# Kernel tuning notes

Measured on AMD Instinct MI355X. Metric: run time of the kernel, lower is better.

## Reference

```python
import jax, jax.numpy as jnp
import numpy as np

BINS = 10          # init kwarg `bins`
LOSS_WEIGHT = 1.0  # init kwarg `loss_weight`


def setup_inputs() -> dict:
    key = jax.random.key(0)
    k1, k2, k3 = jax.random.split(key, 3)
    B, C = 131072, 80  # [batch_num(anchors), class_num]
    pred = jax.random.normal(k1, (B, C), dtype=jnp.float32)
    target = jax.random.randint(k2, (B, C), 0, 2).astype(jnp.int32)
    label_weight = jax.random.randint(k3, (B, C), 0, 2).astype(jnp.int32)
    return {"pred": pred, "target": target, "label_weight": label_weight}


def _ghmc_loss(pred, target_f, valid_f):
    # total number of valid samples (>=1), matches max(valid.sum().item(), 1.0)
    total = jnp.maximum(valid_f.sum(), 1.0)

    # gradient magnitude g = |sigmoid(pred).detach() - target|, in [0, 1]
    g = jnp.abs(jax.nn.sigmoid(jax.lax.stop_gradient(pred)) - target_f)

    # bin index: edges are i/bins, last edge padded by 1e-6, so
    # floor(g * bins) clipped to [0, bins-1] reproduces the torch loop's
    # per-element assignment (elements exactly on an edge take the later bin,
    # matching the sequential overwrite of weights[inds]).
    bin_idx = jnp.clip(jnp.floor(g * BINS).astype(jnp.int32), 0, BINS - 1)

    # histogram of valid elements per bin (invalid routed to extra bin BINS)
    flat_idx = jnp.where(valid_f > 0, bin_idx, BINS).reshape(-1)
    counts = jnp.bincount(flat_idx, length=BINS + 1)[:BINS].astype(pred.dtype)

    # n = number of non-empty bins (>=1 whenever any element is valid)
    n = jnp.maximum((counts > 0).sum(), 1).astype(pred.dtype)

    # per-bin weight total/num_in_bin, zero for empty bins, then /n
    w_bin = jnp.where(counts > 0, total / jnp.maximum(counts, 1.0), 0.0) / n
    weights = jnp.where(valid_f > 0, w_bin[bin_idx], 0.0)
    weights = jax.lax.stop_gradient(weights)  # histogram weights are detached

    # weighted BCE-with-logits, reduction='sum', then / total
    bce = target_f * jax.nn.softplus(-pred) + (1.0 - target_f) * jax.nn.softplus(pred)
    return (weights * bce).sum() / total * LOSS_WEIGHT


def reference(pred, target, label_weight):
    target_f = target.astype(pred.dtype)
    valid_f = (label_weight > 0).astype(pred.dtype)
    return _ghmc_loss(pred, target_f, valid_f)
```

## Files before the change

### kernel.cpp

```cpp
#include <hip/hip_runtime.h>

#define BINS 10
#define TPB  256
#define NB_MAX 2048
#define FTPB 1024

__global__ __launch_bounds__(TPB, 4) void ghmc_hist_kernel(
    const float4* __restrict__ pred4,
    const int4*   __restrict__ tgt4,
    const int4*   __restrict__ lw4,
    float* __restrict__ part,
    int n4, int n)
{
    float acc_s[BINS];
#pragma unroll
    for (int b = 0; b < BINS; ++b) acc_s[b] = 0.f;
    unsigned long long cA = 0ull, cB = 0ull;

    auto proc = [&](float p, int t, int w) {
        float q   = __int_as_float(__float_as_int(p) ^ (int)((unsigned)t << 31));
        float e   = __expf(-fabsf(q));
        float d   = 1.f + e;
        float r   = __builtin_amdgcn_rcpf(d);
        float sig = (q >= 0.f) ? r : e * r;
        int bin   = (int)(sig * 10.f);
        bin = bin > (BINS - 1) ? (BINS - 1) : bin;
        bool valid = (w > 0);
        float bce = fmaxf(q, 0.f) + __logf(d);
        int binm  = valid ? bin : 255;
#pragma unroll
        for (int b = 0; b < BINS; ++b)
            acc_s[b] += (binm == b) ? bce : 0.f;
        unsigned long long inc = valid ? (1ull << (12 * (bin >> 1))) : 0ull;
        bool odd = (bin & 1) != 0;
        cA += odd ? 0ull : inc;
        cB += odd ? inc  : 0ull;
    };

    const int tid    = threadIdx.x;
    const int stride = gridDim.x * TPB;

    int iA = blockIdx.x * TPB + tid;
    bool vA = iA < n4;
    float4 pA; int4 tA, wA;
    if (vA) { pA = pred4[iA]; tA = tgt4[iA]; wA = lw4[iA]; }
    while (vA) {
        const int iB = iA + stride;
        const bool vB = iB < n4;
        float4 pB; int4 tB, wB;
        if (vB) { pB = pred4[iB]; tB = tgt4[iB]; wB = lw4[iB]; }

        proc(pA.x, tA.x, wA.x); proc(pA.y, tA.y, wA.y);
        proc(pA.z, tA.z, wA.z); proc(pA.w, tA.w, wA.w);

        iA = iB + stride;
        vA = iA < n4;
        if (vA) { pA = pred4[iA]; tA = tgt4[iA]; wA = lw4[iA]; }

        if (vB) {
            proc(pB.x, tB.x, wB.x); proc(pB.y, tB.y, wB.y);
            proc(pB.z, tB.z, wB.z); proc(pB.w, tB.w, wB.w);
        }
    }
    {
        const float* predf = (const float*)pred4;
        const int*   tgtf  = (const int*)tgt4;
        const int*   lwf   = (const int*)lw4;
        for (int j = n4 * 4 + blockIdx.x * TPB + tid; j < n; j += stride)
            proc(predf[j], tgtf[j], lwf[j]);
    }

    float cnt[BINS];
#pragma unroll
    for (int b = 0; b < BINS; ++b) {
        unsigned long long pk = (b & 1) ? cB : cA;
        cnt[b] = (float)((pk >> (12 * (b >> 1))) & 0xFFFull);
    }

#pragma unroll
    for (int b = 0; b < BINS; ++b) {
#pragma unroll
        for (int off = 1; off <= 8; off <<= 1) {
            acc_s[b] += __shfl_xor(acc_s[b], off, 64);
            cnt[b]   += __shfl_xor(cnt[b],   off, 64);
        }
    }

    __shared__ float red[2 * BINS][16];
    const int grp = tid >> 4;
    if ((tid & 15) == 0) {
#pragma unroll
        for (int b = 0; b < BINS; ++b) {
            red[b][grp]        = acc_s[b];
            red[BINS + b][grp] = cnt[b];
        }
    }
    __syncthreads();
    if (tid < 2 * BINS) {
        float v = 0.f;
#pragma unroll
        for (int g = 0; g < 16; ++g) v += red[tid][g];
        part[blockIdx.x * (2 * BINS) + tid] = v;
    }
}

__global__ __launch_bounds__(FTPB) void ghmc_final_kernel(
    const float* __restrict__ part, float* __restrict__ out, int nb)
{
    float acc[2 * BINS];
#pragma unroll
    for (int v = 0; v < 2 * BINS; ++v) acc[v] = 0.f;

    const int tid = threadIdx.x;
    for (int i = tid; i < nb; i += FTPB) {
        const float4* rec = (const float4*)(part + (size_t)i * (2 * BINS));
        float4 a = rec[0], b = rec[1], c = rec[2], d = rec[3], e = rec[4];
        acc[0]  += a.x; acc[1]  += a.y; acc[2]  += a.z; acc[3]  += a.w;
        acc[4]  += b.x; acc[5]  += b.y; acc[6]  += b.z; acc[7]  += b.w;
        acc[8]  += c.x; acc[9]  += c.y; acc[10] += c.z; acc[11] += c.w;
        acc[12] += d.x; acc[13] += d.y; acc[14] += d.z; acc[15] += d.w;
        acc[16] += e.x; acc[17] += e.y; acc[18] += e.z; acc[19] += e.w;
    }

#pragma unroll
    for (int v = 0; v < 2 * BINS; ++v) {
#pragma unroll
        for (int off = 1; off <= 32; off <<= 1)
            acc[v] += __shfl_xor(acc[v], off, 64);
    }

    __shared__ float sh[2 * BINS][16];
    const int wv = tid >> 6, lane = tid & 63;
    if (lane == 0) {
#pragma unroll
        for (int v = 0; v < 2 * BINS; ++v) sh[v][wv] = acc[v];
    }
    __syncthreads();
    if (tid < 2 * BINS) {
        float s = 0.f;
#pragma unroll
        for (int g = 0; g < 16; ++g) s += sh[tid][g];
        sh[tid][0] = s;
    }
    __syncthreads();

    if (tid == 0) {
        float ti = 0.f; int nbn = 0;
        float cnts[BINS];
#pragma unroll
        for (int b = 0; b < BINS; ++b) {
            cnts[b] = sh[BINS + b][0];
            ti += cnts[b];
            nbn += (cnts[b] > 0.f) ? 1 : 0;
        }
        float total = fmaxf(ti, 1.f);
        float nf    = (float)(nbn > 0 ? nbn : 1);
        float loss  = 0.f;
#pragma unroll
        for (int b = 0; b < BINS; ++b) {
            if (cnts[b] > 0.f) {
                float w = (total / cnts[b]) / nf;
                loss += w * sh[b][0];
            }
        }
        out[0] = loss / total * 1.0f;
    }
}

extern "C" void kernel_launch(void* const* d_in, const int* in_sizes, int n_in,
                              void* d_out, int out_size, void* d_ws, size_t ws_size,
                              hipStream_t stream)
{
    const float4* pred4 = (const float4*)d_in[0];
    const int4*   tgt4  = (const int4*)d_in[1];
    const int4*   lw4   = (const int4*)d_in[2];

    const int n  = in_sizes[0];
    const int n4 = n / 4;

    int nb = (n4 + TPB - 1) / TPB;
    if (nb > NB_MAX) nb = NB_MAX;
    int ws_cap = (int)(ws_size / (2 * BINS * sizeof(float)));
    if (nb > ws_cap) nb = ws_cap;
    if (nb < 1) nb = 1;

    float* part = (float*)d_ws;

    ghmc_hist_kernel<<<nb, TPB, 0, stream>>>(pred4, tgt4, lw4, part, n4, n);
    ghmc_final_kernel<<<1, FTPB, 0, stream>>>(part, (float*)d_out, nb);
}
```

Baseline: 40.97 us.

## Pack per-bin counts into float sum accumulators and restructure the streaming loop

Each valid element now adds its BCE value plus a 4096 offset into a single per-bin float accumulator. Counts and sums are recovered afterwards by floor-dividing by the offset, which removes the separate 64-bit packed counters and their selects. Bin selection uses a shift-and-mask of the value's bits instead of a compare-select. The grid-stride loop is rewritten with a precomputed iteration count, a software-prefetched body unrolled by two, and single-pass tail handling. The risk is precision: large offsets in a float accumulator lose low-order bits of the BCE sums, and any BCE above 4096 would corrupt the count recovery.

```diff
diff --git a/kernel.cpp b/kernel.cpp
--- a/kernel.cpp
+++ b/kernel.cpp
@@ -4,6 +4,7 @@
 #define TPB  256
 #define NB_MAX 2048
 #define FTPB 1024
+#define KPACK 4096.0f
 
 __global__ __launch_bounds__(TPB, 4) void ghmc_hist_kernel(
     const float4* __restrict__ pred4,
@@ -12,77 +13,82 @@
     float* __restrict__ part,
     int n4, int n)
 {
-    float acc_s[BINS];
+    float acc[BINS];
 #pragma unroll
-    for (int b = 0; b < BINS; ++b) acc_s[b] = 0.f;
-    unsigned long long cA = 0ull, cB = 0ull;
+    for (int b = 0; b < BINS; ++b) acc[b] = 0.f;
 
     auto proc = [&](float p, int t, int w) {
-        float q   = __int_as_float(__float_as_int(p) ^ (int)((unsigned)t << 31));
-        float e   = __expf(-fabsf(q));
-        float d   = 1.f + e;
-        float r   = __builtin_amdgcn_rcpf(d);
-        float sig = (q >= 0.f) ? r : e * r;
-        int bin   = (int)(sig * 10.f);
+        float q    = __int_as_float(__float_as_int(p) ^ (t << 31));
+        float e    = __expf(-fabsf(q));
+        float d    = 1.f + e;
+        float r    = __builtin_amdgcn_rcpf(d);
+        float num  = (q >= 0.f) ? 1.0f : e;
+        float sig10 = num * (10.f * r);
+        int bin    = (int)sig10;
         bin = bin > (BINS - 1) ? (BINS - 1) : bin;
-        bool valid = (w > 0);
-        float bce = fmaxf(q, 0.f) + __logf(d);
-        int binm  = valid ? bin : 255;
+        float bce  = fmaxf(q, 0.f) + __logf(d);
+        float v    = (w > 0) ? (bce + KPACK) : 0.f;
+        int bit    = 1 << bin;
+        int vbits  = __float_as_int(v);
 #pragma unroll
-        for (int b = 0; b < BINS; ++b)
-            acc_s[b] += (binm == b) ? bce : 0.f;
-        unsigned long long inc = valid ? (1ull << (12 * (bin >> 1))) : 0ull;
-        bool odd = (bin & 1) != 0;
-        cA += odd ? 0ull : inc;
-        cB += odd ? inc  : 0ull;
+        for (int b = 0; b < BINS; ++b) {
+            int sel = ((int)((unsigned)bit << (31 - b))) >> 31;
+            acc[b] += __int_as_float(sel & vbits);
+        }
     };
 
     const int tid    = threadIdx.x;
     const int stride = gridDim.x * TPB;
+    const int base   = blockIdx.x * TPB + tid;
 
-    int iA = blockIdx.x * TPB + tid;
-    bool vA = iA < n4;
+    const int full = n4 / stride;
+
+    int i = base;
     float4 pA; int4 tA, wA;
-    if (vA) { pA = pred4[iA]; tA = tgt4[iA]; wA = lw4[iA]; }
-    while (vA) {
-        const int iB = iA + stride;
-        const bool vB = iB < n4;
-        float4 pB; int4 tB, wB;
-        if (vB) { pB = pred4[iB]; tB = tgt4[iB]; wB = lw4[iB]; }
-
+    if (full > 0) { pA = pred4[i]; tA = tgt4[i]; wA = lw4[i]; }
+#pragma unroll 2
+    for (int k = 0; k < full - 1; ++k) {
+        const int j = i + stride;
+        float4 pB = pred4[j]; int4 tB = tgt4[j]; int4 wB = lw4[j];
         proc(pA.x, tA.x, wA.x); proc(pA.y, tA.y, wA.y);
         proc(pA.z, tA.z, wA.z); proc(pA.w, tA.w, wA.w);
-
-        iA = iB + stride;
-        vA = iA < n4;
-        if (vA) { pA = pred4[iA]; tA = tgt4[iA]; wA = lw4[iA]; }
-
-        if (vB) {
-            proc(pB.x, tB.x, wB.x); proc(pB.y, tB.y, wB.y);
-            proc(pB.z, tB.z, wB.z); proc(pB.w, tB.w, wB.w);
+        pA = pB; tA = tB; wA = wB;
+        i = j;
+    }
+    if (full > 0) {
+        proc(pA.x, tA.x, wA.x); proc(pA.y, tA.y, wA.y);
+        proc(pA.z, tA.z, wA.z); proc(pA.w, tA.w, wA.w);
+    }
+    {
+        const int j = base + full * stride;
+        if (j < n4) {
+            float4 p = pred4[j]; int4 t = tgt4[j]; int4 w = lw4[j];
+            proc(p.x, t.x, w.x); proc(p.y, t.y, w.y);
+            proc(p.z, t.z, w.z); proc(p.w, t.w, w.w);
         }
     }
-    {
+    if (blockIdx.x == 0 && tid < (n & 3)) {
         const float* predf = (const float*)pred4;
         const int*   tgtf  = (const int*)tgt4;
         const int*   lwf   = (const int*)lw4;
-        for (int j = n4 * 4 + blockIdx.x * TPB + tid; j < n; j += stride)
-            proc(predf[j], tgtf[j], lwf[j]);
+        const int j = n4 * 4 + tid;
+        proc(predf[j], tgtf[j], lwf[j]);
     }
 
-    float cnt[BINS];
+    float s_[BINS], c_[BINS];
 #pragma unroll
     for (int b = 0; b < BINS; ++b) {
-        unsigned long long pk = (b & 1) ? cB : cA;
-        cnt[b] = (float)((pk >> (12 * (b >> 1))) & 0xFFFull);
+        float Cf = floorf(acc[b] * (1.f / KPACK));
+        c_[b] = Cf;
+        s_[b] = acc[b] - KPACK * Cf;
     }
 
 #pragma unroll
     for (int b = 0; b < BINS; ++b) {
 #pragma unroll
         for (int off = 1; off <= 8; off <<= 1) {
-            acc_s[b] += __shfl_xor(acc_s[b], off, 64);
-            cnt[b]   += __shfl_xor(cnt[b],   off, 64);
+            s_[b] += __shfl_xor(s_[b], off, 64);
+            c_[b] += __shfl_xor(c_[b], off, 64);
         }
     }
 
@@ -91,8 +97,8 @@
     if ((tid & 15) == 0) {
 #pragma unroll
         for (int b = 0; b < BINS; ++b) {
-            red[b][grp]        = acc_s[b];
-            red[BINS + b][grp] = cnt[b];
+            red[b][grp]        = s_[b];
+            red[BINS + b][grp] = c_[b];
         }
     }
     __syncthreads();
```

Result: faster. 38.55 us (-5.9%).
